# Performance work log

Hardware: AMD Instinct MI355X
Metric: run time of the kernel (lower is better)

Reference implementation:

```python
import jax, jax.numpy as jnp
import numpy as np

B, T, D, C, L, H = 8192, 128, 1, 1, 1, 64


def _mlp(x, w1, b1, w2, b2):
    # Linear -> Softplus -> Linear
    return jax.nn.softplus(x @ w1 + b1) @ w2 + b2


def setup_inputs() -> dict:
    key = jax.random.key(0)
    ks = jax.random.split(key, 32)
    s = 0.1

    def w(k, shape):
        return jax.random.normal(k, shape, jnp.float32) * s

    p = {}
    p["xs"] = jax.random.normal(ks[0], (T, B, D), jnp.float32)
    p["ts"] = jnp.arange(T, dtype=jnp.float32)
    p["noise_std"] = jnp.float32(5.0)
    p["eps0"] = jax.random.normal(ks[1], (B, L), jnp.float32)
    p["dW_std"] = jax.random.normal(ks[2], (T - 1, B, L), jnp.float32)
    # encoder: data -> hidden -> context
    p["ew1"] = w(ks[3], (D, H)); p["eb1"] = w(ks[4], (H,))
    p["ew2"] = w(ks[5], (H, C)); p["eb2"] = w(ks[6], (C,))
    # qz0_net: context -> 2*latent
    p["qw"] = w(ks[7], (C, 2 * L)); p["qb"] = w(ks[8], (2 * L,))
    # f_net: latent+context -> hidden -> latent
    p["fw1"] = w(ks[9], (L + C, H)); p["fb1"] = w(ks[10], (H,))
    p["fw2"] = w(ks[11], (H, L)); p["fb2"] = w(ks[12], (L,))
    # h_net: latent -> hidden -> latent
    p["hw1"] = w(ks[13], (L, H)); p["hb1"] = w(ks[14], (H,))
    p["hw2"] = w(ks[15], (H, L)); p["hb2"] = w(ks[16], (L,))
    # g_nets: L independent 1 -> hidden -> 1 -> sigmoid nets, stacked on leading L axis
    p["gw1"] = w(ks[17], (L, H)); p["gb1"] = w(ks[18], (L, H))
    p["gw2"] = w(ks[19], (L, H)); p["gb2"] = w(ks[20], (L,))
    # projector: latent -> hidden -> data
    p["pw1"] = w(ks[21], (L, H)); p["pb1"] = w(ks[22], (H,))
    p["pw2"] = w(ks[23], (H, D)); p["pb2"] = w(ks[24], (D,))
    p["pz0_mean"] = jnp.zeros((1, L), jnp.float32)
    p["pz0_logstd"] = jnp.zeros((1, L), jnp.float32)
    return p


def reference(xs, ts, noise_std, eps0, dW_std,
              ew1, eb1, ew2, eb2, qw, qb,
              fw1, fb1, fw2, fb2, hw1, hb1, hw2, hb2,
              gw1, gb1, gw2, gb2, pw1, pb1, pw2, pb2,
              pz0_mean, pz0_logstd):
    Tn = ts.shape[0]
    # ctx = flip(encoder(flip(xs)))  (encoder is pointwise in time)
    ctx = jnp.flip(_mlp(jnp.flip(xs, axis=0), ew1, eb1, ew2, eb2), axis=0)  # [T,B,C]
    qz = ctx[0] @ qw + qb
    qm, qls = jnp.split(qz, 2, axis=1)  # [B,L] each
    z0 = qm + jnp.exp(qls) * eps0

    def g_fn(z):  # per-coordinate diagonal diffusion nets
        hid = jax.nn.softplus(z[:, :, None] * gw1[None] + gb1[None])  # [B,L,H]
        return jax.nn.sigmoid(jnp.einsum('blh,lh->bl', hid, gw2) + gb2)

    def step(z, inp):
        k, dwk = inp
        t = ts[k]
        dt = ts[k + 1] - ts[k]
        idx = jnp.minimum(jnp.searchsorted(ts, t, side='right'), Tn - 1)
        c = jnp.take(ctx, idx, axis=0)  # [B,C]
        fv = _mlp(jnp.concatenate([z, c], axis=1), fw1, fb1, fw2, fb2)
        hv = _mlp(z, hw1, hb1, hw2, hb2)
        gv = g_fn(z)
        u = (fv - hv) / gv
        lr = 0.5 * jnp.sum(u * u, axis=1) * dt  # logqp path increment [B]
        z_next = z + fv * dt + gv * dwk * jnp.sqrt(dt)  # Euler-Maruyama
        return z_next, (z_next, lr)

    _, (ztail, log_ratio) = jax.lax.scan(step, z0, (jnp.arange(Tn - 1), dW_std))
    zs = jnp.concatenate([z0[None], ztail], axis=0)  # [T,B,L]
    _xs = _mlp(zs, pw1, pb1, pw2, pb2)  # [T,B,D]
    lp = -0.5 * ((xs - _xs) / noise_std) ** 2 - jnp.log(noise_std) - 0.5 * jnp.log(2 * jnp.pi)
    log_pxs = lp.sum(axis=(0, 2)).mean()
    kl = (pz0_logstd - qls) + (jnp.exp(2 * qls) + (qm - pz0_mean) ** 2) / (2 * jnp.exp(2 * pz0_logstd)) - 0.5
    logqp0 = kl.sum(axis=1).mean()
    logqp_path = log_ratio.sum(axis=0).mean()
    return (log_pxs, logqp0 + logqp_path)
```

## Files before the change

kernel.cpp:

```cpp
#include <hip/hip_runtime.h>
#include <math.h>


#define B_SZ 8192
#define T_SZ 128
#define NBLK 32

#define NT1 1025
#define NT2 1025
#define NEE 1024
#define NENT (NT1 + NT2 + NEE)

#define ENT_F4 3
#define MT_FLOATS (4 * ENT_F4 * (NT1 + NT2))
#define T2_BASE4 (ENT_F4 * NT1)
#define ET2G_OFF  MT_FLOATS
#define TABG_FLOATS (MT_FLOATS + 2048)

#define NXI 1024
#define XSF 64.0f
#define XOF 512.0f

#if __has_builtin(__builtin_amdgcn_rcpf)
#define RCPF(x) __builtin_amdgcn_rcpf(x)
#else
#define RCPF(x) (1.0f / (x))
#endif
#if __has_builtin(__builtin_amdgcn_sqrtf)
#define SQRTF(x) __builtin_amdgcn_sqrtf(x)
#else
#define SQRTF(x) sqrtf(x)
#endif

__device__ __forceinline__ float sp_precise(float a) {
  return fmaxf(a, 0.0f) + log1pf(expf(-fabsf(a)));
}
__device__ __forceinline__ float wsum64(float v) {
  #pragma unroll
  for (int m = 1; m <= 32; m <<= 1) v += __shfl_xor(v, m);
  return v;
}

__global__ __launch_bounds__(256) void build_tabs(
    const float* __restrict__ ew1, const float* __restrict__ eb1,
    const float* __restrict__ ew2, const float* __restrict__ eb2,
    const float* __restrict__ fw1, const float* __restrict__ fb1,
    const float* __restrict__ fw2, const float* __restrict__ fb2,
    const float* __restrict__ hw1, const float* __restrict__ hb1,
    const float* __restrict__ hw2, const float* __restrict__ hb2,
    const float* __restrict__ gw1, const float* __restrict__ gb1,
    const float* __restrict__ gw2, const float* __restrict__ gb2,
    const float* __restrict__ pw1, const float* __restrict__ pb1,
    const float* __restrict__ pw2, const float* __restrict__ pb2,
    float* __restrict__ tabs, int* __restrict__ ctr)
{
  const int gtid = blockIdx.x * 256 + threadIdx.x;
  if (gtid == 0) *ctr = 0;
  const int ent  = gtid >> 6;
  const int lane = threadIdx.x & 63;
  if (ent >= NENT) return;

  if (ent < NT1 + NT2) {
    const bool t1 = ent < NT1;
    const int  i  = t1 ? ent : (ent - NT1);
    const float z = t1 ? (-128.0f + (float)i * 0.25f)
                       : (-8192.0f + (float)i * 16.0f);
    const int base4 = (t1 ? 0 : T2_BASE4) + ENT_F4 * i;

    const float az = fmaf(z, fw1[lane], fb1[lane]);
    const float wc = fw1[64 + lane], w2 = fw2[lane];
    float s0 = sp_precise(fmaf(-3.0f, wc, az)) * w2;
    float s1 = sp_precise(fmaf(-1.0f, wc, az)) * w2;
    float s2 = sp_precise(fmaf( 1.0f, wc, az)) * w2;
    float s3 = sp_precise(fmaf( 3.0f, wc, az)) * w2;
    float sh = sp_precise(fmaf(z, hw1[lane], hb1[lane])) * hw2[lane];
    float sg = sp_precise(fmaf(z, gw1[lane], gb1[lane])) * gw2[lane];
    float sp = sp_precise(fmaf(z, pw1[lane], pb1[lane])) * pw2[lane];
    s0 = wsum64(s0); s1 = wsum64(s1); s2 = wsum64(s2); s3 = wsum64(s3);
    sh = wsum64(sh); sg = wsum64(sg); sp = wsum64(sp);
    if (lane == 0) {
      const float fb = fb2[0];
      ((float4*)tabs)[base4]     = make_float4(s0 + fb, s1 + fb, s2 + fb, s3 + fb);
      ((float4*)tabs)[base4 + 1] = make_float4(
          sh + hb2[0],
          1.0f / (1.0f + expf(-(sg + gb2[0]))),
          sp + pb2[0], 0.0f);
      ((float4*)tabs)[base4 + 2] = make_float4(0.f, 0.f, 0.f, 0.f);
    }
  } else {
    const int i = ent - (NT1 + NT2);
    const float x0 = -8.0f + (float)i * (1.0f / 64.0f);
    const float x1 = x0 + (1.0f / 64.0f);
    const float w = ew1[lane], bb = eb1[lane], w2 = ew2[lane];
    float s0 = sp_precise(fmaf(x0, w, bb)) * w2;
    float s1 = sp_precise(fmaf(x1, w, bb)) * w2;
    s0 = wsum64(s0); s1 = wsum64(s1);
    if (lane == 0) {
      const float eb = eb2[0];
      ((float2*)(tabs + ET2G_OFF))[i] = make_float2(s0 + eb, s1 + eb);
    }
  }
}

__global__ __launch_bounds__(256) void ctx_pre(
    const float* __restrict__ xs, const float* __restrict__ tabs,
    float* __restrict__ ctx)
{
  const int i = blockIdx.x * 256 + threadIdx.x;
  const float2* et2 = (const float2*)(tabs + ET2G_OFF);
  const float s = fmaf(xs[i], XSF, XOF);
  const float sc = fminf(fmaxf(s, 0.0f), (float)(NXI - 1));
  const int ii = (int)sc;
  const float fr = s - (float)ii;
  const float2 e = et2[ii];
  ctx[i] = fmaf(fr, e.y - e.x, e.x);
}

__global__ __launch_bounds__(256) void sde_scan(
    const float* __restrict__ xs, const float* __restrict__ ts,
    const float* __restrict__ noise_std, const float* __restrict__ eps0,
    const float* __restrict__ dW, const float* __restrict__ ctx,
    const float* __restrict__ qw,  const float* __restrict__ qb,
    const float* __restrict__ fw1, const float* __restrict__ fb1,
    const float* __restrict__ fw2, const float* __restrict__ fb2,
    const float* __restrict__ hw1, const float* __restrict__ hb1,
    const float* __restrict__ hw2, const float* __restrict__ hb2,
    const float* __restrict__ gw1, const float* __restrict__ gb1,
    const float* __restrict__ gw2, const float* __restrict__ gb2,
    const float* __restrict__ pw1, const float* __restrict__ pb1,
    const float* __restrict__ pw2, const float* __restrict__ pb2,
    const float* __restrict__ pz0_mean, const float* __restrict__ pz0_logstd,
    const float* __restrict__ tabsrc,
    int* __restrict__ ctr, float* __restrict__ partA, float* __restrict__ partB,
    float* __restrict__ out)
{
  __shared__ __align__(16) float tab[MT_FLOATS];
  __shared__ float la[256], lb[256];
  __shared__ int lastflag;

  const int tid = threadIdx.x;
  const int b   = blockIdx.x * 256 + tid;

  {
    const float4* s4 = (const float4*)tabsrc;
    float4* d4 = (float4*)tab;
    for (int i = tid; i < MT_FLOATS / 4; i += 256) d4[i] = s4[i];
  }
  __syncthreads();

  const float4* tab4 = (const float4*)tab;

  const float fb2s = fb2[0], hb2s = hb2[0], gb2s = gb2[0], pb2s = pb2[0];
  const float qw0 = qw[0], qw1 = qw[1], qb0 = qb[0], qb1 = qb[1];
  const float ns = noise_std[0];
  const float inv_ns = 1.0f / ns;
  const float nh_i2 = -0.5f * inv_ns * inv_ns;
  const float pm = pz0_mean[0], pls = pz0_logstd[0];

  auto lagr = [&](float c) {
    const float c2 = c * c;
    const float p1 = c2 - 1.0f, p3 = c2 - 9.0f;
    return make_float4(p1 * (c - 3.0f) * (-1.0f / 48.0f),
                       p3 * (c - 1.0f) * ( 1.0f / 16.0f),
                       p3 * (c + 1.0f) * (-1.0f / 16.0f),
                       p1 * (c + 3.0f) * ( 1.0f / 48.0f));
  };
  auto hgp_exact = [&](float z_, float& hv_, float& gv_, float& pv_) {
    float sh = 0.f, sg = 0.f, sp = 0.f;
    for (int j = 0; j < 64; ++j) {
      sh = fmaf(sp_precise(fmaf(z_, hw1[j], hb1[j])), hw2[j], sh);
      sg = fmaf(sp_precise(fmaf(z_, gw1[j], gb1[j])), gw2[j], sg);
      sp = fmaf(sp_precise(fmaf(z_, pw1[j], pb1[j])), pw2[j], sp);
    }
    hv_ = sh + hb2s;
    gv_ = 1.0f / (1.0f + expf(-(sg + gb2s)));
    pv_ = sp + pb2s;
  };
  auto f_exact = [&](float z_, float c_) {
    float s = 0.f;
    for (int j = 0; j < 64; ++j)
      s = fmaf(sp_precise(fmaf(z_, fw1[j], fmaf(c_, fw1[64 + j], fb1[j]))), fw2[j], s);
    return s + fb2s;
  };
  auto zidx = [&](float z_, int& base4_, float& frac_, bool& inr_) {
    const float s1 = fmaf(z_, 4.0f, 512.0f);
    const float s2 = fmaf(z_, 0.0625f, 512.0f);
    const bool t1 = (s1 >= 0.0f) && (s1 <= 1024.0f);
    const bool t2 = (s2 >= 0.0f) && (s2 <= 1024.0f);
    inr_ = t1 || t2;
    const float sf = t1 ? s1 : fminf(fmaxf(s2, 0.0f), 1024.0f);
    const int fi = min((int)sf, 1023);
    base4_ = (t1 ? 0 : T2_BASE4) + ENT_F4 * fi;
    frac_ = sf - (float)fi;
  };

  const float x0 = xs[b];
  const float c0v = ctx[b];
  const float qm  = fmaf(c0v, qw0, qb0);
  const float qls = fmaf(c0v, qw1, qb1);
  float z = fmaf(__expf(qls), eps0[b], qm);
  const float dqm = qm - pm;
  const float kl = (pls - qls)
                 + (__expf(2.0f * qls) + dqm * dqm) * (0.5f * __expf(-2.0f * pls))
                 - 0.5f;

  float xbuf0 = xs[1 * B_SZ + b], cbuf0 = ctx[1 * B_SZ + b], wbuf0 = dW[0 * B_SZ + b];
  float xbuf1 = xs[2 * B_SZ + b], cbuf1 = ctx[2 * B_SZ + b], wbuf1 = dW[1 * B_SZ + b];
  float xbuf2 = xs[3 * B_SZ + b], cbuf2 = ctx[3 * B_SZ + b], wbuf2 = dW[2 * B_SZ + b];
  float xbuf3 = xs[4 * B_SZ + b], cbuf3 = ctx[4 * B_SZ + b], wbuf3 = dW[3 * B_SZ + b];

  bool zin; int zb4; float zfr;
  float4 q0a, q0b, q1a, q1b;
  float hv, gv, pv;
  zidx(z, zb4, zfr, zin);
  q0a = tab4[zb4]; q0b = tab4[zb4 + 1];
  q1a = tab4[zb4 + ENT_F4]; q1b = tab4[zb4 + ENT_F4 + 1];
  if (zin) {
    hv = fmaf(zfr, q1b.x - q0b.x, q0b.x);
    gv = fmaf(zfr, q1b.y - q0b.y, q0b.y);
    pv = fmaf(zfr, q1b.z - q0b.z, q0b.z);
  } else {
    hgp_exact(z, hv, gv, pv);
  }
  float lp_sum; { const float d = x0 - pv; lp_sum = nh_i2 * d * d; }
  float lr_sum = 0.0f;

#define STEP(K, J) { \
    const float dt = ts[(K) + 1] - ts[(K)]; \
    const float sq = SQRTF(dt); \
    const float cc = cbuf##J; \
    const float4 L = lagr(cc); \
    const bool cin = fabsf(cc) <= 3.0f; \
    float fv; \
    if (zin && cin) { \
      const float n0 = fmaf(zfr, q1a.x - q0a.x, q0a.x); \
      const float n1 = fmaf(zfr, q1a.y - q0a.y, q0a.y); \
      const float n2 = fmaf(zfr, q1a.z - q0a.z, q0a.z); \
      const float n3 = fmaf(zfr, q1a.w - q0a.w, q0a.w); \
      fv = n0 * L.x + n1 * L.y + n2 * L.z + n3 * L.w; \
    } else { \
      fv = f_exact(z, cc); \
    } \
    const float gvs = fmaxf(gv, 1e-6f); \
    const float uu = (fv - hv) * RCPF(gvs); \
    lr_sum = fmaf((0.5f * dt) * uu, uu, lr_sum); \
    z = fmaf(gvs * wbuf##J, sq, fmaf(fv, dt, z)); \
    zidx(z, zb4, zfr, zin); \
    q0a = tab4[zb4]; q0b = tab4[zb4 + 1]; \
    q1a = tab4[zb4 + ENT_F4]; q1b = tab4[zb4 + ENT_F4 + 1]; \
     \
    const int kk_ = (K) + 4; \
    const int ix_ = ((kk_ + 1 < T_SZ) ? kk_ + 1 : T_SZ - 1) * B_SZ + b; \
    const float xb_n = xs[ix_]; \
    const float cb_n = ctx[ix_]; \
    const float wb_n = (kk_ < T_SZ - 1) ? dW[kk_ * B_SZ + b] : 0.0f; \
    if (zin) { \
      hv = fmaf(zfr, q1b.x - q0b.x, q0b.x); \
      gv = fmaf(zfr, q1b.y - q0b.y, q0b.y); \
      pv = fmaf(zfr, q1b.z - q0b.z, q0b.z); \
    } else { \
      hgp_exact(z, hv, gv, pv); \
    } \
    const float d_ = xbuf##J - pv; \
    lp_sum = fmaf(nh_i2 * d_, d_, lp_sum); \
    xbuf##J = xb_n; cbuf##J = cb_n; wbuf##J = wb_n; \
  }

  for (int k = 0; k < 124; k += 4) {
    STEP(k, 0); STEP(k + 1, 1); STEP(k + 2, 2); STEP(k + 3, 3);
  }
  STEP(124, 0); STEP(125, 1); STEP(126, 2);
#undef STEP

  la[tid] = lp_sum; lb[tid] = kl + lr_sum;
  __syncthreads();
  for (int s = 128; s > 0; s >>= 1) {
    if (tid < s) { la[tid] += la[tid + s]; lb[tid] += lb[tid + s]; }
    __syncthreads();
  }
  if (tid == 0) {
    partA[blockIdx.x] = la[0]; partB[blockIdx.x] = lb[0];
    __threadfence();
    lastflag = (atomicAdd(ctr, 1) == NBLK - 1) ? 1 : 0;
  }
  __syncthreads();
  if (lastflag) {
    __threadfence();
    la[tid] = (tid < NBLK) ? partA[tid] : 0.0f;
    lb[tid] = (tid < NBLK) ? partB[tid] : 0.0f;
    __syncthreads();
    for (int s = 128; s > 0; s >>= 1) {
      if (tid < s) { la[tid] += la[tid + s]; lb[tid] += lb[tid + s]; }
      __syncthreads();
    }
    if (tid == 0) {
      out[0] = la[0] / (float)B_SZ
             + (float)T_SZ * (-__logf(ns) - 0.9189385332046727f);
      out[1] = lb[0] / (float)B_SZ;
    }
  }
}

extern "C" void kernel_launch(void* const* d_in, const int* in_sizes, int n_in,
                              void* d_out, int out_size, void* d_ws, size_t ws_size,
                              hipStream_t stream) {
  const float* xs        = (const float*)d_in[0];
  const float* ts        = (const float*)d_in[1];
  const float* noise_std = (const float*)d_in[2];
  const float* eps0      = (const float*)d_in[3];
  const float* dW        = (const float*)d_in[4];
  const float* ew1 = (const float*)d_in[5];
  const float* eb1 = (const float*)d_in[6];
  const float* ew2 = (const float*)d_in[7];
  const float* eb2 = (const float*)d_in[8];
  const float* qw  = (const float*)d_in[9];
  const float* qb  = (const float*)d_in[10];
  const float* fw1 = (const float*)d_in[11];
  const float* fb1 = (const float*)d_in[12];
  const float* fw2 = (const float*)d_in[13];
  const float* fb2 = (const float*)d_in[14];
  const float* hw1 = (const float*)d_in[15];
  const float* hb1 = (const float*)d_in[16];
  const float* hw2 = (const float*)d_in[17];
  const float* hb2 = (const float*)d_in[18];
  const float* gw1 = (const float*)d_in[19];
  const float* gb1 = (const float*)d_in[20];
  const float* gw2 = (const float*)d_in[21];
  const float* gb2 = (const float*)d_in[22];
  const float* pw1 = (const float*)d_in[23];
  const float* pb1 = (const float*)d_in[24];
  const float* pw2 = (const float*)d_in[25];
  const float* pb2 = (const float*)d_in[26];
  const float* pz0_mean   = (const float*)d_in[27];
  const float* pz0_logstd = (const float*)d_in[28];
  float* out = (float*)d_out;

  float* tabs  = (float*)d_ws;
  int*   ctr   = (int*)(tabs + TABG_FLOATS);
  float* partA = tabs + TABG_FLOATS + 4;
  float* partB = partA + NBLK;
  float* ctxb  = tabs + TABG_FLOATS + 72;

  build_tabs<<<(NENT * 64 + 255) / 256, 256, 0, stream>>>(
      ew1, eb1, ew2, eb2, fw1, fb1, fw2, fb2,
      hw1, hb1, hw2, hb2, gw1, gb1, gw2, gb2,
      pw1, pb1, pw2, pb2, tabs, ctr);

  ctx_pre<<<(T_SZ * B_SZ) / 256, 256, 0, stream>>>(xs, tabs, ctxb);

  sde_scan<<<NBLK, 256, 0, stream>>>(
      xs, ts, noise_std, eps0, dW, ctxb, qw, qb,
      fw1, fb1, fw2, fb2, hw1, hb1, hw2, hb2,
      gw1, gb1, gw2, gb2, pw1, pb1, pw2, pb2,
      pz0_mean, pz0_logstd, tabs, ctr, partA, partB, out);
}
```

Before: 61.91 us.

## Split each batch element's SDE scan across 8 lanes with DPP/swizzle reductions

Each batch element is now handled by 8 threads instead of one, so the scan launches 256 blocks instead of 32. Each lane loads one float2 from a repacked 10-float table entry and applies its interpolation and Lagrange weights. Lane shuffles (ds_swizzle and DPP) recombine the f, h, g and p values, and the updated z is broadcast within each lane pair. The goal is more parallelism for this latency-bound sequential loop, since 32 blocks cannot fill the GPU. The cost is extra cross-lane ops and redundant per-lane work, and the exact-evaluation fallback paths are now taken per lane.

```diff
diff --git a/kernel.cpp b/kernel.cpp
--- a/kernel.cpp
+++ b/kernel.cpp
@@ -4,18 +4,18 @@
 
 #define B_SZ 8192
 #define T_SZ 128
-#define NBLK 32
+#define NBLK 256
 
 #define NT1 1025
 #define NT2 1025
 #define NEE 1024
 #define NENT (NT1 + NT2 + NEE)
 
-#define ENT_F4 3
-#define MT_FLOATS (4 * ENT_F4 * (NT1 + NT2))
-#define T2_BASE4 (ENT_F4 * NT1)
-#define ET2G_OFF  MT_FLOATS
-#define TABG_FLOATS (MT_FLOATS + 2048)
+#define ENT_F 10
+#define ZT_FLOATS (ENT_F * (NT1 + NT2))
+#define T2_BASEF (ENT_F * NT1)
+#define ET2G_OFF ZT_FLOATS
+#define TABG_FLOATS (ZT_FLOATS + 2048)
 
 #define NXI 1024
 #define XSF 64.0f
@@ -39,6 +39,14 @@
   #pragma unroll
   for (int m = 1; m <= 32; m <<= 1) v += __shfl_xor(v, m);
   return v;
+}
+__device__ __forceinline__ float swz4(float v) {
+  return __int_as_float(__builtin_amdgcn_ds_swizzle(__float_as_int(v), 0x101F));
+}
+template <int CTRL>
+__device__ __forceinline__ float dpp_mov(float v) {
+  return __int_as_float(
+      __builtin_amdgcn_update_dpp(0, __float_as_int(v), CTRL, 0xF, 0xF, true));
 }
 
 __global__ __launch_bounds__(256) void build_tabs(
@@ -65,7 +73,7 @@
     const int  i  = t1 ? ent : (ent - NT1);
     const float z = t1 ? (-128.0f + (float)i * 0.25f)
                        : (-8192.0f + (float)i * 16.0f);
-    const int base4 = (t1 ? 0 : T2_BASE4) + ENT_F4 * i;
+    const int basef = (t1 ? 0 : T2_BASEF) + ENT_F * i;
 
     const float az = fmaf(z, fw1[lane], fb1[lane]);
     const float wc = fw1[64 + lane], w2 = fw2[lane];
@@ -80,12 +88,16 @@
     sh = wsum64(sh); sg = wsum64(sg); sp = wsum64(sp);
     if (lane == 0) {
       const float fb = fb2[0];
-      ((float4*)tabs)[base4]     = make_float4(s0 + fb, s1 + fb, s2 + fb, s3 + fb);
-      ((float4*)tabs)[base4 + 1] = make_float4(
-          sh + hb2[0],
-          1.0f / (1.0f + expf(-(sg + gb2[0]))),
-          sp + pb2[0], 0.0f);
-      ((float4*)tabs)[base4 + 2] = make_float4(0.f, 0.f, 0.f, 0.f);
+      tabs[basef + 0] = s0 + fb;
+      tabs[basef + 1] = s1 + fb;
+      tabs[basef + 2] = s2 + fb;
+      tabs[basef + 3] = s3 + fb;
+      tabs[basef + 4] = sh + hb2[0];
+      tabs[basef + 5] = 1.0f / (1.0f + expf(-(sg + gb2[0])));
+      tabs[basef + 6] = sp + pb2[0];
+      tabs[basef + 7] = 0.0f;
+      tabs[basef + 8] = 0.0f;
+      tabs[basef + 9] = 0.0f;
     }
   } else {
     const int i = ent - (NT1 + NT2);
@@ -134,21 +146,20 @@
     int* __restrict__ ctr, float* __restrict__ partA, float* __restrict__ partB,
     float* __restrict__ out)
 {
-  __shared__ __align__(16) float tab[MT_FLOATS];
+  __shared__ __align__(16) float tab[ZT_FLOATS];
   __shared__ float la[256], lb[256];
   __shared__ int lastflag;
 
   const int tid = threadIdx.x;
-  const int b   = blockIdx.x * 256 + tid;
+  const int li  = tid & 7;
+  const int b   = blockIdx.x * 32 + (tid >> 3);
 
   {
     const float4* s4 = (const float4*)tabsrc;
     float4* d4 = (float4*)tab;
-    for (int i = tid; i < MT_FLOATS / 4; i += 256) d4[i] = s4[i];
+    for (int i = tid; i < ZT_FLOATS / 4; i += 256) d4[i] = s4[i];
   }
   __syncthreads();
-
-  const float4* tab4 = (const float4*)tab;
 
   const float fb2s = fb2[0], hb2s = hb2[0], gb2s = gb2[0], pb2s = pb2[0];
   const float qw0 = qw[0], qw1 = qw[1], qb0 = qb[0], qb1 = qb[1];
@@ -157,14 +168,6 @@
   const float nh_i2 = -0.5f * inv_ns * inv_ns;
   const float pm = pz0_mean[0], pls = pz0_logstd[0];
 
-  auto lagr = [&](float c) {
-    const float c2 = c * c;
-    const float p1 = c2 - 1.0f, p3 = c2 - 9.0f;
-    return make_float4(p1 * (c - 3.0f) * (-1.0f / 48.0f),
-                       p3 * (c - 1.0f) * ( 1.0f / 16.0f),
-                       p3 * (c + 1.0f) * (-1.0f / 16.0f),
-                       p1 * (c + 3.0f) * ( 1.0f / 48.0f));
-  };
   auto hgp_exact = [&](float z_, float& hv_, float& gv_, float& pv_) {
     float sh = 0.f, sg = 0.f, sp = 0.f;
     for (int j = 0; j < 64; ++j) {
@@ -182,19 +185,18 @@
       s = fmaf(sp_precise(fmaf(z_, fw1[j], fmaf(c_, fw1[64 + j], fb1[j]))), fw2[j], s);
     return s + fb2s;
   };
-  auto zidx = [&](float z_, int& base4_, float& frac_, bool& inr_) {
+  auto zidx = [&](float z_, int& basef_, float& frac_, bool& inr_) {
     const float s1 = fmaf(z_, 4.0f, 512.0f);
-    const float s2 = fmaf(z_, 0.0625f, 512.0f);
+    const float s2v = fmaf(z_, 0.0625f, 512.0f);
     const bool t1 = (s1 >= 0.0f) && (s1 <= 1024.0f);
-    const bool t2 = (s2 >= 0.0f) && (s2 <= 1024.0f);
+    const bool t2 = (s2v >= 0.0f) && (s2v <= 1024.0f);
     inr_ = t1 || t2;
-    const float sf = t1 ? s1 : fminf(fmaxf(s2, 0.0f), 1024.0f);
+    const float sf = t1 ? s1 : fminf(fmaxf(s2v, 0.0f), 1024.0f);
     const int fi = min((int)sf, 1023);
-    base4_ = (t1 ? 0 : T2_BASE4) + ENT_F4 * fi;
+    basef_ = (t1 ? 0 : T2_BASEF) + ENT_F * fi;
     frac_ = sf - (float)fi;
   };
 
-  const float x0 = xs[b];
   const float c0v = ctx[b];
   const float qm  = fmaf(c0v, qw0, qb0);
   const float qls = fmaf(c0v, qw1, qb1);
@@ -204,75 +206,73 @@
                  + (__expf(2.0f * qls) + dqm * dqm) * (0.5f * __expf(-2.0f * pls))
                  - 0.5f;
 
-  float xbuf0 = xs[1 * B_SZ + b], cbuf0 = ctx[1 * B_SZ + b], wbuf0 = dW[0 * B_SZ + b];
-  float xbuf1 = xs[2 * B_SZ + b], cbuf1 = ctx[2 * B_SZ + b], wbuf1 = dW[1 * B_SZ + b];
-  float xbuf2 = xs[3 * B_SZ + b], cbuf2 = ctx[3 * B_SZ + b], wbuf2 = dW[2 * B_SZ + b];
-  float xbuf3 = xs[4 * B_SZ + b], cbuf3 = ctx[4 * B_SZ + b], wbuf3 = dW[3 * B_SZ + b];
-
-  bool zin; int zb4; float zfr;
-  float4 q0a, q0b, q1a, q1b;
-  float hv, gv, pv;
-  zidx(z, zb4, zfr, zin);
-  q0a = tab4[zb4]; q0b = tab4[zb4 + 1];
-  q1a = tab4[zb4 + ENT_F4]; q1b = tab4[zb4 + ENT_F4 + 1];
-  if (zin) {
-    hv = fmaf(zfr, q1b.x - q0b.x, q0b.x);
-    gv = fmaf(zfr, q1b.y - q0b.y, q0b.y);
-    pv = fmaf(zfr, q1b.z - q0b.z, q0b.z);
-  } else {
-    hgp_exact(z, hv, gv, pv);
-  }
-  float lp_sum; { const float d = x0 - pv; lp_sum = nh_i2 * d * d; }
-  float lr_sum = 0.0f;
+  float xbuf0 = xs[0 * B_SZ + b], cbuf0 = ctx[0 * B_SZ + b], wbuf0 = dW[0 * B_SZ + b];
+  float xbuf1 = xs[1 * B_SZ + b], cbuf1 = ctx[1 * B_SZ + b], wbuf1 = dW[1 * B_SZ + b];
+  float xbuf2 = xs[2 * B_SZ + b], cbuf2 = ctx[2 * B_SZ + b], wbuf2 = dW[2 * B_SZ + b];
+  float xbuf3 = xs[3 * B_SZ + b], cbuf3 = ctx[3 * B_SZ + b], wbuf3 = dW[3 * B_SZ + b];
+
+  bool zin; int zb; float zfr;
+  zidx(z, zb, zfr, zin);
+
+  float lrs = 0.0f, lps = 0.0f;
+  const int part = li & 3;
+  const int loff = ((li >> 2) * ENT_F) + 2 * part;
 
 #define STEP(K, J) { \
-    const float dt = ts[(K) + 1] - ts[(K)]; \
+    const int kc = min((K) + 1, T_SZ - 1); \
+    const float dt = ts[kc] - ts[(K)]; \
     const float sq = SQRTF(dt); \
     const float cc = cbuf##J; \
-    const float4 L = lagr(cc); \
+    const float c2 = cc * cc; \
+    const float p1c = c2 - 1.0f, p3c = c2 - 9.0f; \
+    const float L0 = p1c * (cc - 3.0f) * (-1.0f / 48.0f); \
+    const float L1 = p3c * (cc - 1.0f) * ( 1.0f / 16.0f); \
+    const float L2 = p3c * (cc + 1.0f) * (-1.0f / 16.0f); \
+    const float L3 = p1c * (cc + 3.0f) * ( 1.0f / 48.0f); \
     const bool cin = fabsf(cc) <= 3.0f; \
-    float fv; \
-    if (zin && cin) { \
-      const float n0 = fmaf(zfr, q1a.x - q0a.x, q0a.x); \
-      const float n1 = fmaf(zfr, q1a.y - q0a.y, q0a.y); \
-      const float n2 = fmaf(zfr, q1a.z - q0a.z, q0a.z); \
-      const float n3 = fmaf(zfr, q1a.w - q0a.w, q0a.w); \
-      fv = n0 * L.x + n1 * L.y + n2 * L.z + n3 * L.w; \
-    } else { \
-      fv = f_exact(z, cc); \
-    } \
-    const float gvs = fmaxf(gv, 1e-6f); \
-    const float uu = (fv - hv) * RCPF(gvs); \
-    lr_sum = fmaf((0.5f * dt) * uu, uu, lr_sum); \
-    z = fmaf(gvs * wbuf##J, sq, fmaf(fv, dt, z)); \
-    zidx(z, zb4, zfr, zin); \
-    q0a = tab4[zb4]; q0b = tab4[zb4 + 1]; \
-    q1a = tab4[zb4 + ENT_F4]; q1b = tab4[zb4 + ENT_F4 + 1]; \
+    const float2 va = *(const float2*)(tab + zb + loff); \
+    const float wz = (li < 4) ? (1.0f - zfr) : zfr; \
+    const float Asel = (part == 0) ? L0 : ((part == 1) ? L2 : 1.0f); \
+    const float Bsel = (part == 0) ? L1 : ((part == 1) ? L3 : 0.0f); \
+    const float r0 = wz * fmaf(Asel, va.x, Bsel * va.y); \
+    const float r1 = wz * va.y; \
+    const float u0 = r0 + swz4(r0); \
+    const float u1 = r1 + swz4(r1); \
+    const float fv01 = u0 + dpp_mov<0xB1>(u0); \
+    const float X = (part < 2) ? fv01 : u0; \
+    const float xX = dpp_mov<0x4E>(X); \
+    const float xY = dpp_mov<0x4E>(u1); \
+    float FV = (part < 2) ? fv01 : xX; \
+    float HV = (part == 0) ? xX : u0; \
+    float GV = (part == 0) ? xY : u1; \
+    float PV = (part == 1) ? xX : u0; \
+    if (!(zin && cin)) FV = f_exact(z, cc); \
+    if (!zin) { float he, ge, pe; hgp_exact(z, he, ge, pe); HV = he; GV = ge; PV = pe; } \
+    const float gvs = fmaxf(GV, 1e-6f); \
+    const float uu = (FV - HV) * RCPF(gvs); \
+    lrs = fmaf((0.5f * dt) * uu, uu, lrs); \
+    const float zn = fmaf(gvs * wbuf##J, sq, fmaf(FV, dt, z)); \
+    const float znb = dpp_mov<0xB1>(zn); \
+    z = (li & 1) ? znb : zn; \
+    const float d_ = xbuf##J - PV; \
+    lps = fmaf(nh_i2 * d_, d_, lps); \
      \
     const int kk_ = (K) + 4; \
-    const int ix_ = ((kk_ + 1 < T_SZ) ? kk_ + 1 : T_SZ - 1) * B_SZ + b; \
-    const float xb_n = xs[ix_]; \
-    const float cb_n = ctx[ix_]; \
+    const int ixc_ = min(kk_, T_SZ - 1) * B_SZ + b; \
+    const float xb_n = xs[ixc_]; \
+    const float cb_n = ctx[ixc_]; \
     const float wb_n = (kk_ < T_SZ - 1) ? dW[kk_ * B_SZ + b] : 0.0f; \
-    if (zin) { \
-      hv = fmaf(zfr, q1b.x - q0b.x, q0b.x); \
-      gv = fmaf(zfr, q1b.y - q0b.y, q0b.y); \
-      pv = fmaf(zfr, q1b.z - q0b.z, q0b.z); \
-    } else { \
-      hgp_exact(z, hv, gv, pv); \
-    } \
-    const float d_ = xbuf##J - pv; \
-    lp_sum = fmaf(nh_i2 * d_, d_, lp_sum); \
+    zidx(z, zb, zfr, zin); \
     xbuf##J = xb_n; cbuf##J = cb_n; wbuf##J = wb_n; \
   }
 
-  for (int k = 0; k < 124; k += 4) {
+  for (int k = 0; k < T_SZ; k += 4) {
     STEP(k, 0); STEP(k + 1, 1); STEP(k + 2, 2); STEP(k + 3, 3);
   }
-  STEP(124, 0); STEP(125, 1); STEP(126, 2);
 #undef STEP
 
-  la[tid] = lp_sum; lb[tid] = kl + lr_sum;
+  la[tid] = (li == 1) ? lps : 0.0f;
+  lb[tid] = (li == 0) ? (kl + lrs) : 0.0f;
   __syncthreads();
   for (int s = 128; s > 0; s >>= 1) {
     if (tid < s) { la[tid] += la[tid + s]; lb[tid] += lb[tid + s]; }
@@ -286,8 +286,7 @@
   __syncthreads();
   if (lastflag) {
     __threadfence();
-    la[tid] = (tid < NBLK) ? partA[tid] : 0.0f;
-    lb[tid] = (tid < NBLK) ? partB[tid] : 0.0f;
+    la[tid] = partA[tid]; lb[tid] = partB[tid];
     __syncthreads();
     for (int s = 128; s > 0; s >>= 1) {
       if (tid < s) { la[tid] += la[tid + s]; lb[tid] += lb[tid + s]; }
@@ -339,7 +338,7 @@
   int*   ctr   = (int*)(tabs + TABG_FLOATS);
   float* partA = tabs + TABG_FLOATS + 4;
   float* partB = partA + NBLK;
-  float* ctxb  = tabs + TABG_FLOATS + 72;
+  float* ctxb  = partB + NBLK;
 
   build_tabs<<<(NENT * 64 + 255) / 256, 256, 0, stream>>>(
       ew1, eb1, ew2, eb2, fw1, fb1, fw2, fb2,
```

Measured after the change: 66.46 us. 1.07x slower.
